# Optimization experiments

Measured on AMD Instinct MI355X. Metric: run time of the kernel, lower is better.

The kernel has to match this reference:

```python
import jax, jax.numpy as jnp
import numpy as np

NH = 8        # num_heads
KS = 64       # key_size
C_IN = 256
C_OUT = 3 * NH * KS   # 1536
GROUPS = 3 * NH       # 24
EPS = 1e-5
H = W = 64


def setup_inputs() -> dict:
    key = jax.random.key(0)
    k1, k2 = jax.random.split(key)
    x = jax.random.normal(k1, (1, C_IN, H, W), dtype=jnp.float32)
    conv_w = jax.random.normal(k2, (C_OUT, C_IN, 1, 1), dtype=jnp.float32) * 0.05
    gn_w = jnp.ones((C_OUT,), dtype=jnp.float32)
    gn_b = jnp.zeros((C_OUT,), dtype=jnp.float32)
    return {"x": x, "conv_w": conv_w, "gn_w": gn_w, "gn_b": gn_b}


def reference(x, conv_w, gn_w, gn_b):
    B, _, h, w = x.shape
    # 1x1 conv (normalize=True -> no bias): per-pixel GEMM over channels
    attn = jnp.einsum('bchw,oc->bohw', x, conv_w[:, :, 0, 0])  # [B, 1536, H, W]
    # GroupNorm: 24 groups of KS channels, normalized over (KS, H, W)
    g = attn.reshape(B, GROUPS, -1)
    mean = g.mean(axis=-1, keepdims=True)
    var = g.var(axis=-1, keepdims=True)
    g = (g - mean) * jax.lax.rsqrt(var + EPS)
    attn = g.reshape(B, C_OUT, h, w) * gn_w[None, :, None, None] + gn_b[None, :, None, None]
    # split into key, query, value (in that order, per chunk(3, dim=2))
    attn = attn.reshape(B, NH, 3 * KS, h * w)
    key_, query, value = jnp.split(attn, 3, axis=2)   # each [B, NH, KS, HW]
    # saliency = q^T @ k / sqrt(KS) -> [B, NH, HW, HW]
    saliency = jnp.einsum('bnkq,bnkl->bnql', query, key_) / jnp.sqrt(jnp.float32(KS))
    mask = jax.nn.softmax(saliency, axis=-1)
    # out = v @ mask^T -> [B, NH, KS, HW]
    out = jnp.einsum('bnkl,bnql->bnkq', value, mask)
    return out.reshape(B, NH * KS, h, w)
```

## Files before the change

### kernel.cpp

```cpp
#include <hip/hip_runtime.h>

typedef __bf16 bf16;
typedef __bf16 bf16x8 __attribute__((ext_vector_type(8)));
typedef __bf16 bf16x4 __attribute__((ext_vector_type(4)));
typedef float f32x4 __attribute__((ext_vector_type(4)));
typedef float f32x16 __attribute__((ext_vector_type(16)));


#define QF 0.18033688011112042f
#define EXPF(x) __builtin_amdgcn_exp2f(x)

union U4 { bf16x4 v; unsigned u[2]; };
union U8 { bf16x8 v; unsigned u[4]; };

__global__ void k_misc(const float* __restrict__ x, const float* __restrict__ w,
                       bf16* __restrict__ xT, bf16* __restrict__ wb, float* __restrict__ cs) {
    int b = blockIdx.x;
    if (b < 512) {
        int t = b * 256 + threadIdx.x;
        int p  = t & 4095;
        int c0 = (t >> 12) * 8;
        bf16x8 o;
#pragma unroll
        for (int j = 0; j < 8; j++) o[j] = (bf16)x[(c0 + j) * 4096 + p];
        *(bf16x8*)(xT + p * 256 + c0) = o;
    } else if (b < 896) {
        int idx = ((b - 512) * 256 + threadIdx.x) * 4;
        float4 f = *(const float4*)(w + idx);
        bf16x4 o;
        o[0] = (bf16)f.x; o[1] = (bf16)f.y; o[2] = (bf16)f.z; o[3] = (bf16)f.w;
        *(bf16x4*)(wb + idx) = o;
    } else {
#pragma unroll
        for (int i = 0; i < 12; i++) cs[i * 256 + threadIdx.x] = 0.f;
    }
}

__global__ __launch_bounds__(256) void k_conv(const bf16* __restrict__ Wb,
                                              const bf16* __restrict__ xT,
                                              bf16* __restrict__ qkvT,
                                              float* __restrict__ cs) {
    __shared__ __attribute__((aligned(16))) bf16 xs[64 * 72];
    __shared__ __attribute__((aligned(16))) bf16 ws2[64 * 72];
    int wid = threadIdx.x >> 6, lane = threadIdx.x & 63;
    int quad = lane >> 4, l15 = lane & 15;
    int g  = blockIdx.x % 24;
    int pb = (blockIdx.x / 24) * 64;
    int h = g / 3, sec = g % 3;
    int ob = g * 64;

    int srow = threadIdx.x >> 2;
    int scol = (threadIdx.x & 3) * 16;

    f32x4 acc[4];
#pragma unroll
    for (int c = 0; c < 4; c++) acc[c] = (f32x4){0.f, 0.f, 0.f, 0.f};

    bf16x8 fx0 = *(const bf16x8*)(xT + (pb + srow) * 256 + scol);
    bf16x8 fx1 = *(const bf16x8*)(xT + (pb + srow) * 256 + scol + 8);
    bf16x8 fw0 = *(const bf16x8*)(Wb + (ob + srow) * 256 + scol);
    bf16x8 fw1 = *(const bf16x8*)(Wb + (ob + srow) * 256 + scol + 8);

    for (int c4 = 0; c4 < 4; c4++) {
        __syncthreads();
        *(bf16x8*)(xs  + srow * 72 + scol)     = fx0;
        *(bf16x8*)(xs  + srow * 72 + scol + 8) = fx1;
        *(bf16x8*)(ws2 + srow * 72 + scol)     = fw0;
        *(bf16x8*)(ws2 + srow * 72 + scol + 8) = fw1;
        __syncthreads();

        if (c4 < 3) {
            int co = (c4 + 1) * 64;
            fx0 = *(const bf16x8*)(xT + (pb + srow) * 256 + co + scol);
            fx1 = *(const bf16x8*)(xT + (pb + srow) * 256 + co + scol + 8);
            fw0 = *(const bf16x8*)(Wb + (ob + srow) * 256 + co + scol);
            fw1 = *(const bf16x8*)(Wb + (ob + srow) * 256 + co + scol + 8);
        }

#pragma unroll
        for (int k2 = 0; k2 < 2; k2++) {
            bf16x8 a = *(const bf16x8*)(ws2 + (wid * 16 + l15) * 72 + k2 * 32 + quad * 8);
#pragma unroll
            for (int c = 0; c < 4; c++) {
                bf16x8 b = *(const bf16x8*)(xs + (c * 16 + l15) * 72 + k2 * 32 + quad * 8);
                acc[c] = __builtin_amdgcn_mfma_f32_16x16x32_bf16(a, b, acc[c], 0, 0, 0);
            }
        }
    }

    int ch0 = wid * 16 + quad * 4;
#pragma unroll
    for (int r = 0; r < 4; r++) {
        float sp  = acc[0][r] + acc[1][r] + acc[2][r] + acc[3][r];
        float ssp = acc[0][r] * acc[0][r] + acc[1][r] * acc[1][r]
                  + acc[2][r] * acc[2][r] + acc[3][r] * acc[3][r];
#pragma unroll
        for (int m = 1; m < 16; m <<= 1) {
            sp  += __shfl_xor(sp,  m, 64);
            ssp += __shfl_xor(ssp, m, 64);
        }
        if (l15 == 0) {
            atomicAdd(cs + (ob + ch0 + r) * 2,     sp);
            atomicAdd(cs + (ob + ch0 + r) * 2 + 1, ssp);
        }
    }

    __syncthreads();
    bf16* tile = xs;
    if (sec == 2) {
#pragma unroll
        for (int c = 0; c < 4; c++)
#pragma unroll
            for (int r = 0; r < 4; r++)
                tile[(ch0 + r) * 72 + c * 16 + l15] = (bf16)acc[c][r];
    } else {
#pragma unroll
        for (int c = 0; c < 4; c++) {
            bf16x4 o;
#pragma unroll
            for (int r = 0; r < 4; r++) o[r] = (bf16)acc[c][r];
            *(bf16x4*)(&tile[(c * 16 + l15) * 72 + ch0]) = o;
        }
    }
    __syncthreads();
    bf16* base = qkvT + h * 786432;
    int t = threadIdx.x;
    if (sec == 2) {
        bf16* V = base + 524288;
#pragma unroll
        for (int it = 0; it < 2; it++) {
            int e = it * 256 + t; int ch = e >> 3; int pxo = (e & 7) * 8;
            *(bf16x8*)(V + ch * 4096 + pb + pxo) = *(const bf16x8*)(&tile[ch * 72 + pxo]);
        }
    } else {
        bf16* dst = base + (sec == 0 ? 262144 : 0);
#pragma unroll
        for (int it = 0; it < 2; it++) {
            int e = it * 256 + t; int px = e >> 3; int cho = (e & 7) * 8;
            *(bf16x8*)(dst + (pb + px) * 64 + cho) = *(const bf16x8*)(&tile[px * 72 + cho]);
        }
    }
}

#define PF_BLOCK(S, CORR, PFA, PFB)                                             \
    {                                                                           \
        float p0 = EXPF(S[0] + CORR),  p1 = EXPF(S[1] + CORR);                  \
        float p2 = EXPF(S[2] + CORR),  p3 = EXPF(S[3] + CORR);                  \
        float p4 = EXPF(S[4] + CORR),  p5 = EXPF(S[5] + CORR);                  \
        float p6 = EXPF(S[6] + CORR),  p7 = EXPF(S[7] + CORR);                  \
        float p8 = EXPF(S[8] + CORR),  p9 = EXPF(S[9] + CORR);                  \
        float p10 = EXPF(S[10] + CORR), p11 = EXPF(S[11] + CORR);               \
        float p12 = EXPF(S[12] + CORR), p13 = EXPF(S[13] + CORR);               \
        float p14 = EXPF(S[14] + CORR), p15 = EXPF(S[15] + CORR);               \
        lacc += (((p0 + p1) + (p2 + p3)) + ((p4 + p5) + (p6 + p7)))             \
              + (((p8 + p9) + (p10 + p11)) + ((p12 + p13) + (p14 + p15)));      \
        U4 lo, hi;                                                              \
        lo.v[0] = (bf16)p0;  lo.v[1] = (bf16)p1;  lo.v[2] = (bf16)p2;  lo.v[3] = (bf16)p3;  \
        hi.v[0] = (bf16)p4;  hi.v[1] = (bf16)p5;  hi.v[2] = (bf16)p6;  hi.v[3] = (bf16)p7;  \
        unsigned a0 = lo.u[0], b0 = hi.u[0], a1 = lo.u[1], b1 = hi.u[1];        \
        asm("v_permlane32_swap_b32 %0, %1" : "+v"(a0), "+v"(b0));               \
        asm("v_permlane32_swap_b32 %0, %1" : "+v"(a1), "+v"(b1));               \
        U8 fA; fA.u[0] = a0; fA.u[1] = a1; fA.u[2] = b0; fA.u[3] = b1;          \
        PFA = fA.v;                                                             \
        U4 lo2, hi2;                                                            \
        lo2.v[0] = (bf16)p8;  lo2.v[1] = (bf16)p9;  lo2.v[2] = (bf16)p10; lo2.v[3] = (bf16)p11; \
        hi2.v[0] = (bf16)p12; hi2.v[1] = (bf16)p13; hi2.v[2] = (bf16)p14; hi2.v[3] = (bf16)p15; \
        unsigned a2 = lo2.u[0], b2 = hi2.u[0], a3 = lo2.u[1], b3 = hi2.u[1];    \
        asm("v_permlane32_swap_b32 %0, %1" : "+v"(a2), "+v"(b2));               \
        asm("v_permlane32_swap_b32 %0, %1" : "+v"(a3), "+v"(b3));               \
        U8 fB; fB.u[0] = a2; fB.u[1] = a3; fB.u[2] = b2; fB.u[3] = b3;          \
        PFB = fB.v;                                                             \
    }

__global__ __launch_bounds__(256, 4) void k_attn(const bf16* __restrict__ qkvT,
                                                 const float2* __restrict__ cs,
                                                 const float* __restrict__ gnw,
                                                 const float* __restrict__ gnb,
                                                 bf16* __restrict__ Opart,
                                                 float* __restrict__ Lsum) {
    int bid   = blockIdx.x;
    int h     = bid & 7;
    int qb    = (bid >> 3) & 31;
    int split = bid >> 8;
    int wid = threadIdx.x >> 6, lane = threadIdx.x & 63;
    int l31 = lane & 31, half = lane >> 5;
    const bf16* QT = qkvT + h * 786432;
    const bf16* KT = QT + 262144;
    const bf16* V  = QT + 524288;
    int qw = qb * 128 + wid * 32;

    __shared__ __attribute__((aligned(16))) bf16 Ks[2][64 * 72];
    __shared__ __attribute__((aligned(16))) bf16 Vs[2][64 * 72];

    int r0   = threadIdx.x >> 3;
    int koff = (threadIdx.x & 7) * 8;

    float2 vK = cs[(h * 3) * 64 + lane];
    float2 vQ = cs[(h * 3 + 1) * 64 + lane];
    float sK = vK.x, qK = vK.y, sQ = vQ.x, qQ = vQ.y;
#pragma unroll
    for (int m = 1; m < 64; m <<= 1) {
        sK += __shfl_xor(sK, m, 64); qK += __shfl_xor(qK, m, 64);
        sQ += __shfl_xor(sQ, m, 64); qQ += __shfl_xor(qQ, m, 64);
    }
    const float N = 262144.0f;
    float meanK = sK / N, invK = rsqrtf(qK / N - meanK * meanK + 1e-5f);
    float meanQ = sQ / N, invQ = rsqrtf(qQ / N - meanQ * meanQ + 1e-5f);

    float corr = 0.f;
    bf16x8 bq[4];
#pragma unroll
    for (int ks = 0; ks < 4; ks++) {
        bf16x8 raw = *(const bf16x8*)(QT + (qw + l31) * 64 + ks * 16 + half * 8);
#pragma unroll
        for (int j = 0; j < 8; j++) {
            int c = ks * 16 + half * 8 + j;
            float gwq = gnw[h * 192 + 64 + c] * invQ;
            float qv  = (gwq * (float)raw[j] + (gnb[h * 192 + 64 + c] - meanQ * gwq)) * QF;
            float aKc = gnw[h * 192 + c] * invK;
            float bKc = gnb[h * 192 + c] - meanK * aKc;
            corr += bKc * qv;
            bq[ks][j] = (bf16)(aKc * qv);
        }
    }
    corr += __shfl_xor(corr, 32, 64);

    f32x16 oacc0 = (f32x16)(0.0f), oacc1 = (f32x16)(0.0f);
    float ls = 0.f;

    int t0 = split * 16, t1 = t0 + 16;

    bf16x8 kf0, kf1, vf0, vf1;
    {
        int lb0 = t0 * 64;
        kf0 = *(const bf16x8*)(KT + (lb0 + r0) * 64 + koff);
        kf1 = *(const bf16x8*)(KT + (lb0 + r0 + 32) * 64 + koff);
        vf0 = *(const bf16x8*)(V + r0 * 4096 + lb0 + koff);
        vf1 = *(const bf16x8*)(V + (r0 + 32) * 4096 + lb0 + koff);
    }

    for (int lt = t0; lt < t1; lt++) {
        bf16* ksb = Ks[lt & 1];
        bf16* vsb = Vs[lt & 1];

        *(bf16x8*)(ksb + r0 * 72 + koff)        = kf0;
        *(bf16x8*)(ksb + (r0 + 32) * 72 + koff) = kf1;
        *(bf16x8*)(vsb + r0 * 72 + koff)        = vf0;
        *(bf16x8*)(vsb + (r0 + 32) * 72 + koff) = vf1;
        __syncthreads();

        if (lt + 1 < t1) {
            int nb = (lt + 1) * 64;
            kf0 = *(const bf16x8*)(KT + (nb + r0) * 64 + koff);
            kf1 = *(const bf16x8*)(KT + (nb + r0 + 32) * 64 + koff);
            vf0 = *(const bf16x8*)(V + r0 * 4096 + nb + koff);
            vf1 = *(const bf16x8*)(V + (r0 + 32) * 4096 + nb + koff);
        }

        const bf16* ka = ksb + l31 * 72 + half * 8;
        const bf16* kb = ksb + (32 + l31) * 72 + half * 8;
        f32x16 s0 = (f32x16)(0.0f), s1 = (f32x16)(0.0f);
        __builtin_amdgcn_s_setprio(1);
#pragma unroll
        for (int ks = 0; ks < 4; ks++) {
            s0 = __builtin_amdgcn_mfma_f32_32x32x16_bf16(
                *(const bf16x8*)(ka + ks * 16), bq[ks], s0, 0, 0, 0);
            s1 = __builtin_amdgcn_mfma_f32_32x32x16_bf16(
                *(const bf16x8*)(kb + ks * 16), bq[ks], s1, 0, 0, 0);
        }
        __builtin_amdgcn_s_setprio(0);

        float lacc = ls;
        bf16x8 pf0, pf1, pf2, pf3;
        PF_BLOCK(s0, corr, pf0, pf1);
        PF_BLOCK(s1, corr, pf2, pf3);
        ls = lacc;

        const bf16* va = vsb + l31 * 72 + half * 8;
        const bf16* vb = vsb + (32 + l31) * 72 + half * 8;
        __builtin_amdgcn_s_setprio(1);
        oacc0 = __builtin_amdgcn_mfma_f32_32x32x16_bf16(*(const bf16x8*)(va +  0), pf0, oacc0, 0, 0, 0);
        oacc1 = __builtin_amdgcn_mfma_f32_32x32x16_bf16(*(const bf16x8*)(vb +  0), pf0, oacc1, 0, 0, 0);
        oacc0 = __builtin_amdgcn_mfma_f32_32x32x16_bf16(*(const bf16x8*)(va + 16), pf1, oacc0, 0, 0, 0);
        oacc1 = __builtin_amdgcn_mfma_f32_32x32x16_bf16(*(const bf16x8*)(vb + 16), pf1, oacc1, 0, 0, 0);
        oacc0 = __builtin_amdgcn_mfma_f32_32x32x16_bf16(*(const bf16x8*)(va + 32), pf2, oacc0, 0, 0, 0);
        oacc1 = __builtin_amdgcn_mfma_f32_32x32x16_bf16(*(const bf16x8*)(vb + 32), pf2, oacc1, 0, 0, 0);
        oacc0 = __builtin_amdgcn_mfma_f32_32x32x16_bf16(*(const bf16x8*)(va + 48), pf3, oacc0, 0, 0, 0);
        oacc1 = __builtin_amdgcn_mfma_f32_32x32x16_bf16(*(const bf16x8*)(vb + 48), pf3, oacc1, 0, 0, 0);
        __builtin_amdgcn_s_setprio(0);
    }

    ls += __shfl_xor(ls, 32, 64);
    if (half == 0)
        Lsum[split * 32768 + h * 4096 + qw + l31] = ls;

    bf16* Ob = Opart + split * 2097152;
#pragma unroll
    for (int r = 0; r < 16; r++) {
        int kd = (r & 3) + 8 * (r >> 2) + 4 * half;
        Ob[(h * 64 + kd) * 4096 + qw + l31]        = (bf16)oacc0[r];
        Ob[(h * 64 + 32 + kd) * 4096 + qw + l31]   = (bf16)oacc1[r];
    }
}

__global__ void k_final(const bf16* __restrict__ Opart, const float* __restrict__ Lsum,
                        const float2* __restrict__ cs, const float* __restrict__ gnw,
                        const float* __restrict__ gnb, float* __restrict__ out) {
    int gid = blockIdx.x * 256 + threadIdx.x;
    int row = gid >> 9;
    int c8  = (gid & 511) << 3;
    int h   = row >> 6;

    int g = h * 3 + 2;
    int c = threadIdx.x & 63;
    float2 v = cs[g * 64 + c];
    float s = v.x, ss = v.y;
#pragma unroll
    for (int m = 1; m < 64; m <<= 1) { s += __shfl_xor(s, m, 64); ss += __shfl_xor(ss, m, 64); }
    const float N = 262144.0f;
    float mean = s / N;
    float inv  = rsqrtf(ss / N - mean * mean + 1e-5f);
    int gi = h * 192 + 128 + (row & 63);
    float gw = gnw[gi];
    float va = inv * gw;
    float vb = gnb[gi] - mean * inv * gw;

    float o[8] = {0, 0, 0, 0, 0, 0, 0, 0};
    float l[8] = {0, 0, 0, 0, 0, 0, 0, 0};
#pragma unroll
    for (int sp = 0; sp < 4; sp++) {
        bf16x8 vv = *(const bf16x8*)(Opart + sp * 2097152 + row * 4096 + c8);
        const float* L = Lsum + sp * 32768 + h * 4096 + c8;
        float4 l0 = *(const float4*)L;
        float4 l1 = *(const float4*)(L + 4);
#pragma unroll
        for (int j = 0; j < 8; j++) o[j] += (float)vv[j];
        l[0] += l0.x; l[1] += l0.y; l[2] += l0.z; l[3] += l0.w;
        l[4] += l1.x; l[5] += l1.y; l[6] += l1.z; l[7] += l1.w;
    }
    float4 r0, r1;
    r0.x = va * o[0] / l[0] + vb; r0.y = va * o[1] / l[1] + vb;
    r0.z = va * o[2] / l[2] + vb; r0.w = va * o[3] / l[3] + vb;
    r1.x = va * o[4] / l[4] + vb; r1.y = va * o[5] / l[5] + vb;
    r1.z = va * o[6] / l[6] + vb; r1.w = va * o[7] / l[7] + vb;
    *(float4*)(out + row * 4096 + c8)     = r0;
    *(float4*)(out + row * 4096 + c8 + 4) = r1;
}

extern "C" void kernel_launch(void* const* d_in, const int* in_sizes, int n_in,
                              void* d_out, int out_size, void* d_ws, size_t ws_size,
                              hipStream_t stream) {
    const float* x      = (const float*)d_in[0];
    const float* conv_w = (const float*)d_in[1];
    const float* gn_w   = (const float*)d_in[2];
    const float* gn_b   = (const float*)d_in[3];
    float* out = (float*)d_out;
    char* ws = (char*)d_ws;

    bf16*   qkvT  = (bf16*) (ws);
    bf16*   Opart = (bf16*) (ws + 12582912);
    bf16*   Wb    = (bf16*) (ws + 12582912);
    bf16*   xT    = (bf16*) (ws + 13369344);
    float*  Lsum  = (float*)(ws + 29360128);
    float*  cs    = (float*)(ws + 29884416);

    hipLaunchKernelGGL(k_misc,  dim3(897),  dim3(256), 0, stream, x, conv_w, xT, Wb, cs);
    hipLaunchKernelGGL(k_conv,  dim3(1536), dim3(256), 0, stream, Wb, xT, qkvT, cs);
    hipLaunchKernelGGL(k_attn,  dim3(1024), dim3(256), 0, stream, qkvT, (const float2*)cs,
                       gn_w, gn_b, Opart, Lsum);
    hipLaunchKernelGGL(k_final, dim3(1024), dim3(256), 0, stream, Opart, Lsum, (const float2*)cs, gn_w, gn_b, out);
}
```

Before: 137.8 us.

## Load conv operands directly from global and drop softmax per-query bias term

The 1x1-conv kernel no longer stages the weight and input tiles through shared memory with double-buffered register prefetch and barriers. Each wave now reads its MFMA fragments straight from global memory (relying on cache reuse), and the shared buffer is kept only for the output transpose. Separately, the attention kernel drops the per-query correction term from the key GroupNorm bias, since a constant shift of all scores in a row cancels in softmax normalization. This removes an add per score element plus its setup work, but the unnormalized exponentials now run over a different range with no max subtraction, and the conv loads may be less coalesced.

```diff
diff --git a/kernel.cpp b/kernel.cpp
--- a/kernel.cpp
+++ b/kernel.cpp
@@ -40,8 +40,7 @@
                                               const bf16* __restrict__ xT,
                                               bf16* __restrict__ qkvT,
                                               float* __restrict__ cs) {
-    __shared__ __attribute__((aligned(16))) bf16 xs[64 * 72];
-    __shared__ __attribute__((aligned(16))) bf16 ws2[64 * 72];
+    __shared__ __attribute__((aligned(16))) bf16 tile[64 * 72];
     int wid = threadIdx.x >> 6, lane = threadIdx.x & 63;
     int quad = lane >> 4, l15 = lane & 15;
     int g  = blockIdx.x % 24;
@@ -49,42 +48,21 @@
     int h = g / 3, sec = g % 3;
     int ob = g * 64;
 
-    int srow = threadIdx.x >> 2;
-    int scol = (threadIdx.x & 3) * 16;
-
     f32x4 acc[4];
 #pragma unroll
     for (int c = 0; c < 4; c++) acc[c] = (f32x4){0.f, 0.f, 0.f, 0.f};
 
-    bf16x8 fx0 = *(const bf16x8*)(xT + (pb + srow) * 256 + scol);
-    bf16x8 fx1 = *(const bf16x8*)(xT + (pb + srow) * 256 + scol + 8);
-    bf16x8 fw0 = *(const bf16x8*)(Wb + (ob + srow) * 256 + scol);
-    bf16x8 fw1 = *(const bf16x8*)(Wb + (ob + srow) * 256 + scol + 8);
-
-    for (int c4 = 0; c4 < 4; c4++) {
-        __syncthreads();
-        *(bf16x8*)(xs  + srow * 72 + scol)     = fx0;
-        *(bf16x8*)(xs  + srow * 72 + scol + 8) = fx1;
-        *(bf16x8*)(ws2 + srow * 72 + scol)     = fw0;
-        *(bf16x8*)(ws2 + srow * 72 + scol + 8) = fw1;
-        __syncthreads();
-
-        if (c4 < 3) {
-            int co = (c4 + 1) * 64;
-            fx0 = *(const bf16x8*)(xT + (pb + srow) * 256 + co + scol);
-            fx1 = *(const bf16x8*)(xT + (pb + srow) * 256 + co + scol + 8);
-            fw0 = *(const bf16x8*)(Wb + (ob + srow) * 256 + co + scol);
-            fw1 = *(const bf16x8*)(Wb + (ob + srow) * 256 + co + scol + 8);
-        }
-
-#pragma unroll
-        for (int k2 = 0; k2 < 2; k2++) {
-            bf16x8 a = *(const bf16x8*)(ws2 + (wid * 16 + l15) * 72 + k2 * 32 + quad * 8);
-#pragma unroll
-            for (int c = 0; c < 4; c++) {
-                bf16x8 b = *(const bf16x8*)(xs + (c * 16 + l15) * 72 + k2 * 32 + quad * 8);
-                acc[c] = __builtin_amdgcn_mfma_f32_16x16x32_bf16(a, b, acc[c], 0, 0, 0);
-            }
+    const bf16* arow = Wb + (ob + wid * 16 + l15) * 256 + quad * 8;
+    const bf16* brow = xT + (pb + l15) * 256 + quad * 8;
+
+#pragma unroll
+    for (int kc = 0; kc < 8; kc++) {
+        int ko = kc * 32;
+        bf16x8 a = *(const bf16x8*)(arow + ko);
+#pragma unroll
+        for (int c = 0; c < 4; c++) {
+            bf16x8 b = *(const bf16x8*)(brow + c * 16 * 256 + ko);
+            acc[c] = __builtin_amdgcn_mfma_f32_16x16x32_bf16(a, b, acc[c], 0, 0, 0);
         }
     }
 
@@ -105,8 +83,6 @@
         }
     }
 
-    __syncthreads();
-    bf16* tile = xs;
     if (sec == 2) {
 #pragma unroll
         for (int c = 0; c < 4; c++)
@@ -142,16 +118,12 @@
     }
 }
 
-#define PF_BLOCK(S, CORR, PFA, PFB)                                             \
+#define PF_BLOCK(S, PFA, PFB)                                                   \
     {                                                                           \
-        float p0 = EXPF(S[0] + CORR),  p1 = EXPF(S[1] + CORR);                  \
-        float p2 = EXPF(S[2] + CORR),  p3 = EXPF(S[3] + CORR);                  \
-        float p4 = EXPF(S[4] + CORR),  p5 = EXPF(S[5] + CORR);                  \
-        float p6 = EXPF(S[6] + CORR),  p7 = EXPF(S[7] + CORR);                  \
-        float p8 = EXPF(S[8] + CORR),  p9 = EXPF(S[9] + CORR);                  \
-        float p10 = EXPF(S[10] + CORR), p11 = EXPF(S[11] + CORR);               \
-        float p12 = EXPF(S[12] + CORR), p13 = EXPF(S[13] + CORR);               \
-        float p14 = EXPF(S[14] + CORR), p15 = EXPF(S[15] + CORR);               \
+        float p0 = EXPF(S[0]),  p1 = EXPF(S[1]),  p2 = EXPF(S[2]),  p3 = EXPF(S[3]);   \
+        float p4 = EXPF(S[4]),  p5 = EXPF(S[5]),  p6 = EXPF(S[6]),  p7 = EXPF(S[7]);   \
+        float p8 = EXPF(S[8]),  p9 = EXPF(S[9]),  p10 = EXPF(S[10]), p11 = EXPF(S[11]); \
+        float p12 = EXPF(S[12]), p13 = EXPF(S[13]), p14 = EXPF(S[14]), p15 = EXPF(S[15]); \
         lacc += (((p0 + p1) + (p2 + p3)) + ((p4 + p5) + (p6 + p7)))             \
               + (((p8 + p9) + (p10 + p11)) + ((p12 + p13) + (p14 + p15)));      \
         U4 lo, hi;                                                              \
@@ -207,7 +179,6 @@
     float meanK = sK / N, invK = rsqrtf(qK / N - meanK * meanK + 1e-5f);
     float meanQ = sQ / N, invQ = rsqrtf(qQ / N - meanQ * meanQ + 1e-5f);
 
-    float corr = 0.f;
     bf16x8 bq[4];
 #pragma unroll
     for (int ks = 0; ks < 4; ks++) {
@@ -218,12 +189,9 @@
             float gwq = gnw[h * 192 + 64 + c] * invQ;
             float qv  = (gwq * (float)raw[j] + (gnb[h * 192 + 64 + c] - meanQ * gwq)) * QF;
             float aKc = gnw[h * 192 + c] * invK;
-            float bKc = gnb[h * 192 + c] - meanK * aKc;
-            corr += bKc * qv;
             bq[ks][j] = (bf16)(aKc * qv);
         }
     }
-    corr += __shfl_xor(corr, 32, 64);
 
     f32x16 oacc0 = (f32x16)(0.0f), oacc1 = (f32x16)(0.0f);
     float ls = 0.f;
@@ -272,8 +240,8 @@
 
         float lacc = ls;
         bf16x8 pf0, pf1, pf2, pf3;
-        PF_BLOCK(s0, corr, pf0, pf1);
-        PF_BLOCK(s1, corr, pf2, pf3);
+        PF_BLOCK(s0, pf0, pf1);
+        PF_BLOCK(s1, pf2, pf3);
         ls = lacc;
 
         const bf16* va = vsb + l31 * 72 + half * 8;
```

Result: slower. 148.6 us (+7.9%).
